# Performance work log

Measured on AMD Instinct MI355X. Metric: run time of the kernel, lower is better.

The kernel has to match this reference:

```python
import jax, jax.numpy as jnp
import numpy as np

INPUT_DIM = 256
EMBED_DIM = 256
NUM_HEADS = 8
HEAD_DIM = EMBED_DIM // NUM_HEADS
N_TOKENS = 11136
N_BATCH = 16


def _xavier(key, shape):
    fan_out, fan_in = shape
    bound = np.sqrt(6.0 / (fan_in + fan_out)).astype(np.float32)
    return jax.random.uniform(key, shape, jnp.float32, -bound, bound)


def setup_inputs() -> dict:
    key = jax.random.key(0)
    k_x, k_ids, k_qkv, k_o = jax.random.split(key, 4)
    x = jax.random.normal(k_x, (N_TOKENS, INPUT_DIM), jnp.float32)
    batch_ids = jnp.sort(jax.random.randint(k_ids, (N_TOKENS,), 0, N_BATCH)).astype(jnp.int32)
    qkv_w = _xavier(k_qkv, (3 * EMBED_DIM, INPUT_DIM))
    qkv_b = jnp.zeros((3 * EMBED_DIM,), jnp.float32)
    o_w = _xavier(k_o, (EMBED_DIM, EMBED_DIM))
    o_b = jnp.zeros((EMBED_DIM,), jnp.float32)
    return {"x": x, "batch_ids": batch_ids, "qkv_w": qkv_w, "qkv_b": qkv_b,
            "o_w": o_w, "o_b": o_b}


def reference(x, batch_ids, qkv_w, qkv_b, o_w, o_b):
    # batch_ids is concrete metadata (mirrors np.unique on CPU in the original).
    ids = np.asarray(batch_ids)
    vals, counts = np.unique(ids, return_counts=True)
    B = len(vals)
    S = int(counts.max())
    offsets = np.concatenate([np.zeros(1, np.int64), np.cumsum(counts)[:-1]])
    seg = np.searchsorted(vals, ids)               # segment index per token
    pos = np.arange(ids.shape[0]) - offsets[seg]   # position within segment

    qkv = x @ qkv_w.T + qkv_b                      # [N, 3E]
    # pad_sequence with padding_value=1 -> scatter tokens into an all-ones buffer
    fin = jnp.ones((B, S, 3 * EMBED_DIM), qkv.dtype).at[seg, pos].set(qkv)
    # padded rows sum to exactly 3E (all ones) -> mask True marks padding
    pad_mask = fin.sum(-1) >= fin.shape[-1]        # [B, S]

    qkv4 = fin.reshape(B, S, NUM_HEADS, 3 * HEAD_DIM).transpose(0, 2, 1, 3)
    q, k, v = jnp.split(qkv4, 3, axis=-1)          # each [B, H, S, hd]

    logits = jnp.einsum('bhqd,bhkd->bhqk', q, k) * (HEAD_DIM ** -0.5)
    logits = jnp.where(pad_mask[:, None, None, :], -jnp.inf, logits)
    attn = jax.nn.softmax(logits, axis=-1)         # [B, H, S, S]

    out = jnp.einsum('bhqk,bhkd->bhqd', attn, v)
    out = out.transpose(0, 2, 1, 3).reshape(B, S, EMBED_DIM)
    out = out[seg, pos]                            # unpad -> [N, E]
    return out @ o_w.T + o_b
```

## Files before the change

### kernel.cpp

```cpp
#include <hip/hip_runtime.h>
#include <stdint.h>


#define N_TOK 11136
#define E 256
#define H 8
#define HD 32

typedef __attribute__((ext_vector_type(8))) __bf16 bf16x8;
typedef __attribute__((ext_vector_type(8))) unsigned short u16x8;
typedef __attribute__((ext_vector_type(4))) float f32x4;

__device__ __forceinline__ unsigned short f2bf(float f) {
  unsigned int u = __float_as_uint(f);
  u = (u + 0x7FFFu + ((u >> 16) & 1u)) >> 16;
  return (unsigned short)u;
}
__device__ __forceinline__ float bf2f(unsigned short s) {
  return __uint_as_float(((unsigned int)s) << 16);
}
__device__ __forceinline__ bf16x8 ld8(const unsigned short* p) {
  return *(const bf16x8*)p;
}

__global__ void k_offsets(const int* __restrict__ ids, int* __restrict__ offs) {
  int b = threadIdx.x;
  if (b > 16) return;
  int lo = 0, hi = N_TOK;
  while (lo < hi) { int mid = (lo + hi) >> 1; if (ids[mid] < b) lo = mid + 1; else hi = mid; }
  offs[b] = lo;
}

#define QK_BSTRIDE 264
#define QSCALE (0.17677669529663687f * 1.4426950408889634f)
__global__ __launch_bounds__(256, 2) void k_qkv(
    const float* __restrict__ x, const float* __restrict__ qw,
    const float* __restrict__ qkv_b,
    unsigned short* __restrict__ Qb, unsigned short* __restrict__ Kb,
    unsigned short* __restrict__ Vt) {
  __shared__ unsigned short Bhi[48 * QK_BSTRIDE];
  __shared__ unsigned short Blo[48 * QK_BSTRIDE];
  int tid = threadIdx.x;
  int w = tid >> 6, lane = tid & 63, m = lane & 15, quad = lane >> 4;
  int col0 = blockIdx.y * 48;

  {
    const float4* qw4 = (const float4*)(qw + (size_t)col0 * E);
#pragma unroll
    for (int i = 0; i < 12; ++i) {
      int flat = i * 256 + tid;
      float4 v = qw4[flat];
      int row = flat >> 6, kq = flat & 63;
      ushort4 hv, lv;
      hv.x = f2bf(v.x); lv.x = f2bf(v.x - bf2f(hv.x));
      hv.y = f2bf(v.y); lv.y = f2bf(v.y - bf2f(hv.y));
      hv.z = f2bf(v.z); lv.z = f2bf(v.z - bf2f(hv.z));
      hv.w = f2bf(v.w); lv.w = f2bf(v.w - bf2f(hv.w));
      *(ushort4*)(Bhi + row * QK_BSTRIDE + kq * 4) = hv;
      *(ushort4*)(Blo + row * QK_BSTRIDE + kq * 4) = lv;
    }
  }
  __syncthreads();

  int base = blockIdx.x * 192 + w * 48;
  f32x4 acc[3][3] = {};
  for (int kc = 0; kc < 8; ++kc) {
    int ko = kc * 32 + quad * 8;
    bf16x8 ah[3], al[3];
#pragma unroll
    for (int mt = 0; mt < 3; ++mt) {
      const float* ap = x + (size_t)(base + mt * 16 + m) * E + ko;
      float4 u0 = *(const float4*)ap;
      float4 u1 = *(const float4*)(ap + 4);
      float vv[8] = {u0.x, u0.y, u0.z, u0.w, u1.x, u1.y, u1.z, u1.w};
      u16x8 hr, lr_;
#pragma unroll
      for (int i = 0; i < 8; ++i) {
        unsigned short hh = f2bf(vv[i]);
        hr[i] = hh;
        lr_[i] = f2bf(vv[i] - bf2f(hh));
      }
      ah[mt] = __builtin_bit_cast(bf16x8, hr);
      al[mt] = __builtin_bit_cast(bf16x8, lr_);
    }
#pragma unroll
    for (int t = 0; t < 3; ++t) {
      bf16x8 bh = ld8(Bhi + (16 * t + m) * QK_BSTRIDE + ko);
      bf16x8 bl = ld8(Blo + (16 * t + m) * QK_BSTRIDE + ko);
#pragma unroll
      for (int mt = 0; mt < 3; ++mt) {
        acc[mt][t] = __builtin_amdgcn_mfma_f32_16x16x32_bf16(ah[mt], bh, acc[mt][t], 0, 0, 0);
        acc[mt][t] = __builtin_amdgcn_mfma_f32_16x16x32_bf16(ah[mt], bl, acc[mt][t], 0, 0, 0);
        acc[mt][t] = __builtin_amdgcn_mfma_f32_16x16x32_bf16(al[mt], bh, acc[mt][t], 0, 0, 0);
      }
    }
  }
#pragma unroll
  for (int t = 0; t < 3; ++t) {
    int j = col0 + 16 * t + m;
    int hd = j / 96;
    int rr = j - hd * 96;
    float bias = qkv_b[j];
#pragma unroll
    for (int mt = 0; mt < 3; ++mt) {
      int tokb = base + mt * 16 + quad * 4;
      if (rr < 64) {
        float qsc = (rr < 32) ? QSCALE : 1.0f;
        unsigned short* dst = (rr < 32) ? (Qb + (size_t)hd * N_TOK * HD + rr)
                                        : (Kb + (size_t)hd * N_TOK * HD + (rr - 32));
#pragma unroll
        for (int r = 0; r < 4; ++r)
          dst[(size_t)(tokb + r) * HD] = f2bf((acc[mt][t][r] + bias) * qsc);
      } else {
        int d = rr - 64;
        ushort4 pk;
        pk.x = f2bf(acc[mt][t][0] + bias); pk.y = f2bf(acc[mt][t][1] + bias);
        pk.z = f2bf(acc[mt][t][2] + bias); pk.w = f2bf(acc[mt][t][3] + bias);
        *(ushort4*)(Vt + (size_t)(hd * HD + d) * N_TOK + tokb) = pk;
      }
    }
  }
}

#define PSTRIDE 72
__global__ __launch_bounds__(256) void k_attn(
    const int* __restrict__ ids, const int* __restrict__ offs,
    const unsigned short* __restrict__ Qb, const unsigned short* __restrict__ Kb,
    const unsigned short* __restrict__ Vt,
    unsigned short* __restrict__ attnb) {
  __shared__ unsigned short ldsP[4][16 * PSTRIDE];
  int tid = threadIdx.x;
  int w = tid >> 6, lane = tid & 63;
  int m = lane & 15, quad = lane >> 4;
  int h = blockIdx.y;
  int q0 = (blockIdx.x * 4 + w) * 16;
  unsigned short* P = ldsP[w];
  int tok = q0 + m;
  int b = ids[tok];
  int st = offs[b], en = offs[b + 1];
  int kmin = st, kmax = en, stM = st, enm = en;
#pragma unroll
  for (int d = 1; d <= 8; d <<= 1) {
    kmin = min(kmin, __shfl_xor(kmin, d));
    kmax = max(kmax, __shfl_xor(kmax, d));
    stM  = max(stM,  __shfl_xor(stM,  d));
    enm  = min(enm,  __shfl_xor(enm,  d));
  }
  const unsigned short* Kbase = Kb + (size_t)h * N_TOK * HD;
  const unsigned short* Vb0 = Vt + (size_t)(h * HD + m) * N_TOK;
  const unsigned short* Vb1 = Vt + (size_t)(h * HD + 16 + m) * N_TOK;
  bf16x8 qf = ld8(Qb + (size_t)(h * N_TOK + tok) * HD + quad * 8);
  int k0beg = kmin & ~63;

  float lsum = 0.f;
  f32x4 o0 = {}, o1 = {};
  bf16x8 kn[4];
#pragma unroll
  for (int i = 0; i < 4; ++i)
    kn[i] = ld8(Kbase + (size_t)(k0beg + 16 * i + m) * HD + quad * 8);

  for (int k0 = k0beg; k0 < kmax; k0 += 64) {
    bf16x8 kc[4];
#pragma unroll
    for (int i = 0; i < 4; ++i) kc[i] = kn[i];
    int k1 = (k0 + 64 < kmax) ? k0 + 64 : k0;
#pragma unroll
    for (int i = 0; i < 4; ++i)
      kn[i] = ld8(Kbase + (size_t)(k1 + 16 * i + m) * HD + quad * 8);
    bf16x8 vf0[2], vf1[2];
#pragma unroll
    for (int c = 0; c < 2; ++c) {
      vf0[c] = ld8(Vb0 + k0 + 32 * c + quad * 8);
      vf1[c] = ld8(Vb1 + k0 + 32 * c + quad * 8);
    }
    f32x4 s[4];
#pragma unroll
    for (int i = 0; i < 4; ++i) {
      f32x4 z = {};
      s[i] = __builtin_amdgcn_mfma_f32_16x16x32_bf16(kc[i], qf, z, 0, 0, 0);
    }
    bool interior = (k0 >= stM && k0 + 64 <= enm);
    int jb = k0 + quad * 4;
#pragma unroll
    for (int i = 0; i < 4; ++i) {
      float p[4];
#pragma unroll
      for (int r = 0; r < 4; ++r) {
        float sv = s[i][r];
        if (!interior) {
          int j = jb + 16 * i + r;
          bool ok = (j >= st) && (j < en);
          sv = ok ? sv : -3e38f;
        }
        p[r] = exp2f(sv);
      }
      lsum += (p[0] + p[1]) + (p[2] + p[3]);
      unsigned int b0 = __float_as_uint(p[0]) + 0x8000u;
      unsigned int b1 = __float_as_uint(p[1]) + 0x8000u;
      unsigned int b2 = __float_as_uint(p[2]) + 0x8000u;
      unsigned int b3 = __float_as_uint(p[3]) + 0x8000u;
      uint2 pk;
      pk.x = (b1 & 0xFFFF0000u) | (b0 >> 16);
      pk.y = (b3 & 0xFFFF0000u) | (b2 >> 16);
      *(uint2*)(P + m * PSTRIDE + 16 * i + quad * 4) = pk;
    }
#pragma unroll
    for (int c = 0; c < 2; ++c) {
      bf16x8 pf = ld8(P + m * PSTRIDE + 32 * c + quad * 8);
      o0 = __builtin_amdgcn_mfma_f32_16x16x32_bf16(vf0[c], pf, o0, 0, 0, 0);
      o1 = __builtin_amdgcn_mfma_f32_16x16x32_bf16(vf1[c], pf, o1, 0, 0, 0);
    }
  }
  lsum += __shfl_xor(lsum, 16);
  lsum += __shfl_xor(lsum, 32);
  float inv = 1.0f / lsum;
  ushort4 pk0, pk1;
  pk0.x = f2bf(o0[0] * inv); pk0.y = f2bf(o0[1] * inv);
  pk0.z = f2bf(o0[2] * inv); pk0.w = f2bf(o0[3] * inv);
  pk1.x = f2bf(o1[0] * inv); pk1.y = f2bf(o1[1] * inv);
  pk1.z = f2bf(o1[2] * inv); pk1.w = f2bf(o1[3] * inv);
  *(ushort4*)(attnb + (size_t)tok * E + h * HD + quad * 4) = pk0;
  *(ushort4*)(attnb + (size_t)tok * E + h * HD + 16 + quad * 4) = pk1;
}

__global__ __launch_bounds__(256, 2) void k_oproj(
    const unsigned short* __restrict__ attnb, const float* __restrict__ ow,
    const float* __restrict__ ob, float* __restrict__ out) {
  __shared__ unsigned short Bo[64 * QK_BSTRIDE];
  int tid = threadIdx.x;
  int w = tid >> 6, lane = tid & 63, m = lane & 15, quad = lane >> 4;
  int tok0 = blockIdx.x * 64, col0 = blockIdx.y * 64;
  {
    const float4* ow4 = (const float4*)(ow + (size_t)col0 * E);
#pragma unroll
    for (int i = 0; i < 16; ++i) {
      int flat = i * 256 + tid;
      float4 v = ow4[flat];
      int row = flat >> 6, kq = flat & 63;
      ushort4 hv;
      hv.x = f2bf(v.x); hv.y = f2bf(v.y); hv.z = f2bf(v.z); hv.w = f2bf(v.w);
      *(ushort4*)(Bo + row * QK_BSTRIDE + kq * 4) = hv;
    }
  }
  __syncthreads();
  f32x4 acc[4] = {};
  int arow = tok0 + 16 * w + m;
  for (int kc = 0; kc < 8; ++kc) {
    int ko = kc * 32 + quad * 8;
    bf16x8 a = ld8(attnb + (size_t)arow * E + ko);
#pragma unroll
    for (int t = 0; t < 4; ++t) {
      bf16x8 b = ld8(Bo + (16 * t + m) * QK_BSTRIDE + ko);
      acc[t] = __builtin_amdgcn_mfma_f32_16x16x32_bf16(a, b, acc[t], 0, 0, 0);
    }
  }
#pragma unroll
  for (int t = 0; t < 4; ++t) {
    int j = col0 + 16 * t + m;
    float bias = ob[j];
#pragma unroll
    for (int r = 0; r < 4; ++r) {
      int tok = tok0 + 16 * w + quad * 4 + r;
      out[(size_t)tok * E + j] = acc[t][r] + bias;
    }
  }
}

extern "C" void kernel_launch(void* const* d_in, const int* in_sizes, int n_in,
                              void* d_out, int out_size, void* d_ws, size_t ws_size,
                              hipStream_t stream) {
  const float* x   = (const float*)d_in[0];
  const int*   ids = (const int*)d_in[1];
  const float* qw  = (const float*)d_in[2];
  const float* qb  = (const float*)d_in[3];
  const float* ow  = (const float*)d_in[4];
  const float* ob  = (const float*)d_in[5];
  float* out = (float*)d_out;

  char* p = (char*)d_ws;
  auto alloc = [&](size_t bytes) {
    char* r = p;
    p += (bytes + 255) & ~(size_t)255;
    return r;
  };
  int* offs = (int*)alloc(32 * sizeof(int));
  unsigned short* Qb  = (unsigned short*)alloc((size_t)N_TOK * E * 2);
  unsigned short* Kb  = (unsigned short*)alloc((size_t)N_TOK * E * 2);
  unsigned short* Vt  = (unsigned short*)alloc((size_t)N_TOK * E * 2);
  unsigned short* att = (unsigned short*)alloc((size_t)N_TOK * E * 2);

  k_offsets<<<dim3(1), dim3(64), 0, stream>>>(ids, offs);
  k_qkv<<<dim3(N_TOK / 192, 16), dim3(256), 0, stream>>>(x, qw, qb, Qb, Kb, Vt);
  k_attn<<<dim3(N_TOK / 64, H), dim3(256), 0, stream>>>(ids, offs, Qb, Kb, Vt, att);
  k_oproj<<<dim3(N_TOK / 64, E / 64), dim3(256), 0, stream>>>(att, ow, ob, out);
}
```

Measured before the change: 186.7 us.

## Share K/V tiles via double-buffered LDS in attention; shrink QKV GEMM tiles

The attention kernel now has all four waves of a block cooperatively load each 64-key K and V tile into double-buffered shared memory. Before, each wave fetched the tiles from global memory on its own. The key range becomes the union across the block, and a block barrier is added per iteration. The QKV projection kernel drops from 48 to 16 tokens per wave, which gives three times as many blocks, a higher occupancy hint and register prefetch of the next x chunk. It also swaps exp2f for a raw v_exp_f32. The costs are more redundant weight staging per block in the projection, extra barriers, and possibly more masked key tiles when a block spans segments.

```diff
diff --git a/kernel.cpp b/kernel.cpp
--- a/kernel.cpp
+++ b/kernel.cpp
@@ -33,13 +33,13 @@
 
 #define QK_BSTRIDE 264
 #define QSCALE (0.17677669529663687f * 1.4426950408889634f)
-__global__ __launch_bounds__(256, 2) void k_qkv(
+__global__ __launch_bounds__(256, 3) void k_qkv(
     const float* __restrict__ x, const float* __restrict__ qw,
     const float* __restrict__ qkv_b,
     unsigned short* __restrict__ Qb, unsigned short* __restrict__ Kb,
     unsigned short* __restrict__ Vt) {
-  __shared__ unsigned short Bhi[48 * QK_BSTRIDE];
-  __shared__ unsigned short Blo[48 * QK_BSTRIDE];
+  __shared__ __align__(16) unsigned short Bhi[48 * QK_BSTRIDE];
+  __shared__ __align__(16) unsigned short Blo[48 * QK_BSTRIDE];
   int tid = threadIdx.x;
   int w = tid >> 6, lane = tid & 63, m = lane & 15, quad = lane >> 4;
   int col0 = blockIdx.y * 48;
@@ -62,37 +62,35 @@
   }
   __syncthreads();
 
-  int base = blockIdx.x * 192 + w * 48;
-  f32x4 acc[3][3] = {};
+  int base = blockIdx.x * 64 + w * 16;
+  const float* ap = x + (size_t)(base + m) * E;
+  f32x4 acc[3] = {};
+  float4 c0 = *(const float4*)(ap + quad * 8);
+  float4 c1 = *(const float4*)(ap + quad * 8 + 4);
   for (int kc = 0; kc < 8; ++kc) {
+    float4 u0 = c0, u1 = c1;
+    if (kc < 7) {
+      c0 = *(const float4*)(ap + (kc + 1) * 32 + quad * 8);
+      c1 = *(const float4*)(ap + (kc + 1) * 32 + quad * 8 + 4);
+    }
     int ko = kc * 32 + quad * 8;
-    bf16x8 ah[3], al[3];
-#pragma unroll
-    for (int mt = 0; mt < 3; ++mt) {
-      const float* ap = x + (size_t)(base + mt * 16 + m) * E + ko;
-      float4 u0 = *(const float4*)ap;
-      float4 u1 = *(const float4*)(ap + 4);
-      float vv[8] = {u0.x, u0.y, u0.z, u0.w, u1.x, u1.y, u1.z, u1.w};
-      u16x8 hr, lr_;
-#pragma unroll
-      for (int i = 0; i < 8; ++i) {
-        unsigned short hh = f2bf(vv[i]);
-        hr[i] = hh;
-        lr_[i] = f2bf(vv[i] - bf2f(hh));
-      }
-      ah[mt] = __builtin_bit_cast(bf16x8, hr);
-      al[mt] = __builtin_bit_cast(bf16x8, lr_);
-    }
+    float vv[8] = {u0.x, u0.y, u0.z, u0.w, u1.x, u1.y, u1.z, u1.w};
+    u16x8 hr, lr_;
+#pragma unroll
+    for (int i = 0; i < 8; ++i) {
+      unsigned short hh = f2bf(vv[i]);
+      hr[i] = hh;
+      lr_[i] = f2bf(vv[i] - bf2f(hh));
+    }
+    bf16x8 ah = __builtin_bit_cast(bf16x8, hr);
+    bf16x8 al = __builtin_bit_cast(bf16x8, lr_);
 #pragma unroll
     for (int t = 0; t < 3; ++t) {
       bf16x8 bh = ld8(Bhi + (16 * t + m) * QK_BSTRIDE + ko);
       bf16x8 bl = ld8(Blo + (16 * t + m) * QK_BSTRIDE + ko);
-#pragma unroll
-      for (int mt = 0; mt < 3; ++mt) {
-        acc[mt][t] = __builtin_amdgcn_mfma_f32_16x16x32_bf16(ah[mt], bh, acc[mt][t], 0, 0, 0);
-        acc[mt][t] = __builtin_amdgcn_mfma_f32_16x16x32_bf16(ah[mt], bl, acc[mt][t], 0, 0, 0);
-        acc[mt][t] = __builtin_amdgcn_mfma_f32_16x16x32_bf16(al[mt], bh, acc[mt][t], 0, 0, 0);
-      }
+      acc[t] = __builtin_amdgcn_mfma_f32_16x16x32_bf16(ah, bh, acc[t], 0, 0, 0);
+      acc[t] = __builtin_amdgcn_mfma_f32_16x16x32_bf16(ah, bl, acc[t], 0, 0, 0);
+      acc[t] = __builtin_amdgcn_mfma_f32_16x16x32_bf16(al, bh, acc[t], 0, 0, 0);
     }
   }
 #pragma unroll
@@ -101,39 +99,40 @@
     int hd = j / 96;
     int rr = j - hd * 96;
     float bias = qkv_b[j];
-#pragma unroll
-    for (int mt = 0; mt < 3; ++mt) {
-      int tokb = base + mt * 16 + quad * 4;
-      if (rr < 64) {
-        float qsc = (rr < 32) ? QSCALE : 1.0f;
-        unsigned short* dst = (rr < 32) ? (Qb + (size_t)hd * N_TOK * HD + rr)
-                                        : (Kb + (size_t)hd * N_TOK * HD + (rr - 32));
-#pragma unroll
-        for (int r = 0; r < 4; ++r)
-          dst[(size_t)(tokb + r) * HD] = f2bf((acc[mt][t][r] + bias) * qsc);
-      } else {
-        int d = rr - 64;
-        ushort4 pk;
-        pk.x = f2bf(acc[mt][t][0] + bias); pk.y = f2bf(acc[mt][t][1] + bias);
-        pk.z = f2bf(acc[mt][t][2] + bias); pk.w = f2bf(acc[mt][t][3] + bias);
-        *(ushort4*)(Vt + (size_t)(hd * HD + d) * N_TOK + tokb) = pk;
-      }
+    int tokb = base + quad * 4;
+    if (rr < 64) {
+      float qsc = (rr < 32) ? QSCALE : 1.0f;
+      unsigned short* dst = (rr < 32) ? (Qb + (size_t)hd * N_TOK * HD + rr)
+                                      : (Kb + (size_t)hd * N_TOK * HD + (rr - 32));
+#pragma unroll
+      for (int r = 0; r < 4; ++r)
+        dst[(size_t)(tokb + r) * HD] = f2bf((acc[t][r] + bias) * qsc);
+    } else {
+      int d = rr - 64;
+      ushort4 pk;
+      pk.x = f2bf(acc[t][0] + bias); pk.y = f2bf(acc[t][1] + bias);
+      pk.z = f2bf(acc[t][2] + bias); pk.w = f2bf(acc[t][3] + bias);
+      *(ushort4*)(Vt + (size_t)(hd * HD + d) * N_TOK + tokb) = pk;
     }
   }
 }
 
 #define PSTRIDE 72
-__global__ __launch_bounds__(256) void k_attn(
+__global__ __launch_bounds__(256, 4) void k_attn(
     const int* __restrict__ ids, const int* __restrict__ offs,
     const unsigned short* __restrict__ Qb, const unsigned short* __restrict__ Kb,
     const unsigned short* __restrict__ Vt,
     unsigned short* __restrict__ attnb) {
-  __shared__ unsigned short ldsP[4][16 * PSTRIDE];
+  __shared__ __align__(16) unsigned short Kl[2][64 * 32];
+  __shared__ __align__(16) unsigned short Vl[2][32 * 64];
+  __shared__ __align__(16) unsigned short ldsP[4][16 * PSTRIDE];
+  __shared__ int bred[8];
   int tid = threadIdx.x;
   int w = tid >> 6, lane = tid & 63;
   int m = lane & 15, quad = lane >> 4;
   int h = blockIdx.y;
-  int q0 = (blockIdx.x * 4 + w) * 16;
+  int tok0 = blockIdx.x * 64;
+  int q0 = tok0 + w * 16;
   unsigned short* P = ldsP[w];
   int tok = q0 + m;
   int b = ids[tok];
@@ -146,38 +145,42 @@
     stM  = max(stM,  __shfl_xor(stM,  d));
     enm  = min(enm,  __shfl_xor(enm,  d));
   }
-  const unsigned short* Kbase = Kb + (size_t)h * N_TOK * HD;
-  const unsigned short* Vb0 = Vt + (size_t)(h * HD + m) * N_TOK;
-  const unsigned short* Vb1 = Vt + (size_t)(h * HD + 16 + m) * N_TOK;
+  if (lane == 0) { bred[w] = kmin; bred[4 + w] = kmax; }
+  __syncthreads();
+  int kminB = min(min(bred[0], bred[1]), min(bred[2], bred[3]));
+  int kmaxB = max(max(bred[4], bred[5]), max(bred[6], bred[7]));
+  int k0beg = kminB & ~63;
+
+  const unsigned short* Kbase = Qb ? Kb + (size_t)h * N_TOK * HD : Kb;
+  const unsigned short* Vbase = Vt + (size_t)h * HD * N_TOK;
   bf16x8 qf = ld8(Qb + (size_t)(h * N_TOK + tok) * HD + quad * 8);
-  int k0beg = kmin & ~63;
+
+  int krow = w * 16 + (lane >> 2);
+  int kgof = (lane & 3) * 8;
+  int vrow = w * 8 + (lane >> 3);
+  int vgof = (lane & 7) * 8;
+
+  bf16x8 kg = ld8(Kbase + (size_t)(k0beg + krow) * HD + kgof);
+  bf16x8 vg = ld8(Vbase + (size_t)vrow * N_TOK + k0beg + vgof);
+  *(bf16x8*)(&Kl[0][krow * 32 + kgof]) = kg;
+  *(bf16x8*)(&Vl[0][vrow * 64 + vgof]) = vg;
+  __syncthreads();
 
   float lsum = 0.f;
   f32x4 o0 = {}, o1 = {};
-  bf16x8 kn[4];
-#pragma unroll
-  for (int i = 0; i < 4; ++i)
-    kn[i] = ld8(Kbase + (size_t)(k0beg + 16 * i + m) * HD + quad * 8);
-
-  for (int k0 = k0beg; k0 < kmax; k0 += 64) {
-    bf16x8 kc[4];
-#pragma unroll
-    for (int i = 0; i < 4; ++i) kc[i] = kn[i];
-    int k1 = (k0 + 64 < kmax) ? k0 + 64 : k0;
-#pragma unroll
-    for (int i = 0; i < 4; ++i)
-      kn[i] = ld8(Kbase + (size_t)(k1 + 16 * i + m) * HD + quad * 8);
-    bf16x8 vf0[2], vf1[2];
-#pragma unroll
-    for (int c = 0; c < 2; ++c) {
-      vf0[c] = ld8(Vb0 + k0 + 32 * c + quad * 8);
-      vf1[c] = ld8(Vb1 + k0 + 32 * c + quad * 8);
-    }
+  int buf = 0;
+  for (int k0 = k0beg; k0 < kmaxB; k0 += 64) {
+    int k1 = (k0 + 64 < kmaxB) ? (k0 + 64) : k0;
+    kg = ld8(Kbase + (size_t)(k1 + krow) * HD + kgof);
+    vg = ld8(Vbase + (size_t)vrow * N_TOK + k1 + vgof);
+    const unsigned short* Kc = &Kl[buf][0];
+    const unsigned short* Vc = &Vl[buf][0];
     f32x4 s[4];
 #pragma unroll
     for (int i = 0; i < 4; ++i) {
+      bf16x8 kf = ld8(Kc + (16 * i + m) * 32 + quad * 8);
       f32x4 z = {};
-      s[i] = __builtin_amdgcn_mfma_f32_16x16x32_bf16(kc[i], qf, z, 0, 0, 0);
+      s[i] = __builtin_amdgcn_mfma_f32_16x16x32_bf16(kf, qf, z, 0, 0, 0);
     }
     bool interior = (k0 >= stM && k0 + 64 <= enm);
     int jb = k0 + quad * 4;
@@ -189,10 +192,11 @@
         float sv = s[i][r];
         if (!interior) {
           int j = jb + 16 * i + r;
-          bool ok = (j >= st) && (j < en);
-          sv = ok ? sv : -3e38f;
+          sv = (j >= st && j < en) ? sv : -3e38f;
         }
-        p[r] = exp2f(sv);
+        float e;
+        asm("v_exp_f32 %0, %1" : "=v"(e) : "v"(sv));
+        p[r] = e;
       }
       lsum += (p[0] + p[1]) + (p[2] + p[3]);
       unsigned int b0 = __float_as_uint(p[0]) + 0x8000u;
@@ -206,10 +210,16 @@
     }
 #pragma unroll
     for (int c = 0; c < 2; ++c) {
-      bf16x8 pf = ld8(P + m * PSTRIDE + 32 * c + quad * 8);
-      o0 = __builtin_amdgcn_mfma_f32_16x16x32_bf16(vf0[c], pf, o0, 0, 0, 0);
-      o1 = __builtin_amdgcn_mfma_f32_16x16x32_bf16(vf1[c], pf, o1, 0, 0, 0);
-    }
+      bf16x8 pf  = ld8(P + m * PSTRIDE + 32 * c + quad * 8);
+      bf16x8 vf0 = ld8(Vc + m * 64 + 32 * c + quad * 8);
+      bf16x8 vf1 = ld8(Vc + (16 + m) * 64 + 32 * c + quad * 8);
+      o0 = __builtin_amdgcn_mfma_f32_16x16x32_bf16(vf0, pf, o0, 0, 0, 0);
+      o1 = __builtin_amdgcn_mfma_f32_16x16x32_bf16(vf1, pf, o1, 0, 0, 0);
+    }
+    *(bf16x8*)(&Kl[buf ^ 1][krow * 32 + kgof]) = kg;
+    *(bf16x8*)(&Vl[buf ^ 1][vrow * 64 + vgof]) = vg;
+    __syncthreads();
+    buf ^= 1;
   }
   lsum += __shfl_xor(lsum, 16);
   lsum += __shfl_xor(lsum, 32);
@@ -226,7 +236,7 @@
 __global__ __launch_bounds__(256, 2) void k_oproj(
     const unsigned short* __restrict__ attnb, const float* __restrict__ ow,
     const float* __restrict__ ob, float* __restrict__ out) {
-  __shared__ unsigned short Bo[64 * QK_BSTRIDE];
+  __shared__ __align__(16) unsigned short Bo[64 * QK_BSTRIDE];
   int tid = threadIdx.x;
   int w = tid >> 6, lane = tid & 63, m = lane & 15, quad = lane >> 4;
   int tok0 = blockIdx.x * 64, col0 = blockIdx.y * 64;
@@ -290,7 +300,7 @@
   unsigned short* att = (unsigned short*)alloc((size_t)N_TOK * E * 2);
 
   k_offsets<<<dim3(1), dim3(64), 0, stream>>>(ids, offs);
-  k_qkv<<<dim3(N_TOK / 192, 16), dim3(256), 0, stream>>>(x, qw, qb, Qb, Kb, Vt);
+  k_qkv<<<dim3(N_TOK / 64, 16), dim3(256), 0, stream>>>(x, qw, qb, Qb, Kb, Vt);
   k_attn<<<dim3(N_TOK / 64, H), dim3(256), 0, stream>>>(ids, offs, Qb, Kb, Vt, att);
   k_oproj<<<dim3(N_TOK / 64, E / 64), dim3(256), 0, stream>>>(att, ow, ob, out);
 }
```

New measurement: 163.2 us. 12.6% less time.
